# Optimization experiments

Measured on AMD Instinct MI355X. Metric: run time of the kernel, lower is better.

The kernel has to match this reference:

```python
import jax, jax.numpy as jnp
import numpy as np

B, N, D = 64, 1024, 1024

def setup_inputs() -> dict:
    key = jax.random.key(0)
    k1, k2, k3, k4, k5 = jax.random.split(key, 5)
    s = 1.0 / np.sqrt(D)
    return {
        "h_t": jax.random.normal(k1, (B, D), dtype=jnp.float32),
        "keys": jax.random.normal(k2, (B, N, D), dtype=jnp.float32),
        "W_h": jax.random.uniform(k3, (D, D), jnp.float32, -s, s),
        "W_k": jax.random.uniform(k4, (D, D), jnp.float32, -s, s),
        "v": jax.random.uniform(k5, (D,), jnp.float32, -s, s),
    }

def reference(h_t, keys, W_h, W_k, v):
    # W_h(h_t): [B, D]; W_k(keys): [B, N, D]  (nn.Linear computes x @ W.T)
    qh = h_t @ W_h.T                       # [B, D]
    kh = jnp.einsum('bnd,ed->bne', keys, W_k)  # [B, N, D]
    energy = jnp.tanh(qh[:, None, :] + kh)     # [B, N, D]
    scores = jnp.einsum('bnd,d->bn', energy, v)  # [B, N]
    alpha = jax.nn.softmax(scores, axis=-1)      # [B, N]
    context = jnp.einsum('bn,bnd->bd', alpha, keys)  # [B, D]
    return (context, alpha)
```

## Files before the change

### kernel.cpp

```cpp
#include <hip/hip_runtime.h>
#include <math.h>

#define BB 64
#define NN 1024
#define DD 1024

typedef __bf16 bf16x8 __attribute__((ext_vector_type(8)));
typedef float f32x4 __attribute__((ext_vector_type(4)));
typedef unsigned short u16x8 __attribute__((ext_vector_type(8)));

__device__ __forceinline__ float fast_tanh(float x) {
    return 1.f - 2.f / (__expf(2.f * x) + 1.f);
}

__global__ __launch_bounds__(256) void qh_kernel(const float* __restrict__ h_t,
                                                 const float* __restrict__ W_h,
                                                 float* __restrict__ qh,
                                                 float* __restrict__ scores) {
    __shared__ float hs[DD];
    const int b = blockIdx.y;
    const int e = blockIdx.x * 256 + threadIdx.x;
    scores[(blockIdx.y * 4 + blockIdx.x) * 256 + threadIdx.x] = 0.f;
    for (int i = threadIdx.x; i < DD; i += 256) hs[i] = h_t[b * DD + i];
    __syncthreads();
    const float4* wrow = (const float4*)(W_h + (size_t)e * DD);
    float acc = 0.f;
#pragma unroll 4
    for (int k4 = 0; k4 < DD / 4; ++k4) {
        float4 w = wrow[k4];
        acc = fmaf(w.x, hs[4 * k4 + 0], acc);
        acc = fmaf(w.y, hs[4 * k4 + 1], acc);
        acc = fmaf(w.z, hs[4 * k4 + 2], acc);
        acc = fmaf(w.w, hs[4 * k4 + 3], acc);
    }
    qh[b * DD + e] = acc;
}

#define SPAD 40

__device__ __forceinline__ void split16(const float4* __restrict__ src,
                                        unsigned short* hi, unsigned short* lo) {
    float x[16];
    float4 v0 = src[0], v1 = src[1], v2 = src[2], v3 = src[3];
    x[0] = v0.x; x[1] = v0.y; x[2] = v0.z; x[3] = v0.w;
    x[4] = v1.x; x[5] = v1.y; x[6] = v1.z; x[7] = v1.w;
    x[8] = v2.x; x[9] = v2.y; x[10] = v2.z; x[11] = v2.w;
    x[12] = v3.x; x[13] = v3.y; x[14] = v3.z; x[15] = v3.w;
#pragma unroll
    for (int i = 0; i < 16; ++i) {
        unsigned int u = __float_as_uint(x[i]);
        hi[i] = (unsigned short)(u >> 16);
        float hif = __uint_as_float(u & 0xFFFF0000u);
        float lof = x[i] - hif;
        lo[i] = (unsigned short)(__float_as_uint(lof) >> 16);
    }
}

__global__ __launch_bounds__(256, 2) void scores_kernel(const float* __restrict__ keys,
                                                        const float* __restrict__ W_k,
                                                        const float* __restrict__ v,
                                                        const float* __restrict__ qh,
                                                        float* __restrict__ scores) {
    __shared__ unsigned short Ah[128 * SPAD];
    __shared__ unsigned short Al[128 * SPAD];
    __shared__ unsigned short Bh[128 * SPAD];
    __shared__ unsigned short Bl[128 * SPAD];
    __shared__ float vs[128];
    __shared__ float qs[128];
    __shared__ float red[128][2];

    const int tid = threadIdx.x;
    const int cp = blockIdx.x;
    const int rt = blockIdx.y;
    const int b = rt >> 3;
    const int n0 = (rt & 7) * 128;
    const int e0 = cp * 128;

    if (tid < 128) {
        vs[tid] = v[e0 + tid];
        qs[tid] = qh[b * DD + e0 + tid];
    }

    const float* Ag = keys + ((size_t)b * NN + n0) * DD;
    const float* Bg = W_k + (size_t)e0 * DD;

    const int w = tid >> 6;
    const int lane = tid & 63;
    const int wm = w & 1;
    const int we = w >> 1;
    const int lcol = lane & 15;
    const int quad = lane >> 4;

    f32x4 acc[4][4];
#pragma unroll
    for (int mi = 0; mi < 4; ++mi)
#pragma unroll
        for (int ni = 0; ni < 4; ++ni) acc[mi][ni] = (f32x4){0.f, 0.f, 0.f, 0.f};

    const int srow = tid >> 1;
    const int sseg = tid & 1;

    float4 pa[4], pb[4];
    {
        const float4* as = (const float4*)(Ag + (size_t)srow * DD + sseg * 16);
        const float4* bs = (const float4*)(Bg + (size_t)srow * DD + sseg * 16);
#pragma unroll
        for (int i = 0; i < 4; ++i) { pa[i] = as[i]; pb[i] = bs[i]; }
    }

    for (int kt = 0; kt < DD / 32; ++kt) {
        __syncthreads();
        {
            unsigned short hi[16], lo[16];
            split16(pa, hi, lo);
            u16x8* dh = (u16x8*)&Ah[srow * SPAD + sseg * 16];
            u16x8* dl = (u16x8*)&Al[srow * SPAD + sseg * 16];
            dh[0] = *(u16x8*)&hi[0]; dh[1] = *(u16x8*)&hi[8];
            dl[0] = *(u16x8*)&lo[0]; dl[1] = *(u16x8*)&lo[8];
            split16(pb, hi, lo);
            u16x8* eh = (u16x8*)&Bh[srow * SPAD + sseg * 16];
            u16x8* el = (u16x8*)&Bl[srow * SPAD + sseg * 16];
            eh[0] = *(u16x8*)&hi[0]; eh[1] = *(u16x8*)&hi[8];
            el[0] = *(u16x8*)&lo[0]; el[1] = *(u16x8*)&lo[8];
        }
        if (kt + 1 < DD / 32) {
            const int k0 = (kt + 1) * 32;
            const float4* as = (const float4*)(Ag + (size_t)srow * DD + k0 + sseg * 16);
            const float4* bs = (const float4*)(Bg + (size_t)srow * DD + k0 + sseg * 16);
#pragma unroll
            for (int i = 0; i < 4; ++i) { pa[i] = as[i]; pb[i] = bs[i]; }
        }
        __syncthreads();

        bf16x8 ah[4], al[4], bh[4], bl[4];
#pragma unroll
        for (int mi = 0; mi < 4; ++mi) {
            const int r = wm * 64 + mi * 16 + lcol;
            ah[mi] = *(const bf16x8*)&Ah[r * SPAD + quad * 8];
            al[mi] = *(const bf16x8*)&Al[r * SPAD + quad * 8];
        }
#pragma unroll
        for (int ni = 0; ni < 4; ++ni) {
            const int r = we * 64 + ni * 16 + lcol;
            bh[ni] = *(const bf16x8*)&Bh[r * SPAD + quad * 8];
            bl[ni] = *(const bf16x8*)&Bl[r * SPAD + quad * 8];
        }
#pragma unroll
        for (int mi = 0; mi < 4; ++mi)
#pragma unroll
            for (int ni = 0; ni < 4; ++ni) {
                acc[mi][ni] = __builtin_amdgcn_mfma_f32_16x16x32_bf16(ah[mi], bh[ni], acc[mi][ni], 0, 0, 0);
                acc[mi][ni] = __builtin_amdgcn_mfma_f32_16x16x32_bf16(ah[mi], bl[ni], acc[mi][ni], 0, 0, 0);
                acc[mi][ni] = __builtin_amdgcn_mfma_f32_16x16x32_bf16(al[mi], bh[ni], acc[mi][ni], 0, 0, 0);
            }
    }

    float part[4][4];
#pragma unroll
    for (int mi = 0; mi < 4; ++mi)
#pragma unroll
        for (int r = 0; r < 4; ++r) part[mi][r] = 0.f;
#pragma unroll
    for (int mi = 0; mi < 4; ++mi)
#pragma unroll
        for (int ni = 0; ni < 4; ++ni) {
            const int e = we * 64 + ni * 16 + lcol;
            const float vv = vs[e];
            const float qv = qs[e];
#pragma unroll
            for (int r = 0; r < 4; ++r)
                part[mi][r] += vv * fast_tanh(qv + acc[mi][ni][r]);
        }
#pragma unroll
    for (int mi = 0; mi < 4; ++mi)
#pragma unroll
        for (int r = 0; r < 4; ++r) {
            float p = part[mi][r];
            p += __shfl_xor(p, 1);
            p += __shfl_xor(p, 2);
            p += __shfl_xor(p, 4);
            p += __shfl_xor(p, 8);
            if (lcol == 0) red[wm * 64 + mi * 16 + quad * 4 + r][we] = p;
        }
    __syncthreads();
    if (tid < 128) atomicAdd(&scores[b * NN + n0 + tid], red[tid][0] + red[tid][1]);
}

__global__ __launch_bounds__(256) void softmax_kernel(const float* __restrict__ scores,
                                                      float* __restrict__ alpha,
                                                      float* __restrict__ context) {
    const int b = blockIdx.x;
    const int t = threadIdx.x;
#pragma unroll
    for (int j = 0; j < 4; ++j) context[b * DD + t + 256 * j] = 0.f;

    float x[4];
    float m = -1e30f;
#pragma unroll
    for (int j = 0; j < 4; ++j) {
        x[j] = scores[b * NN + t + 256 * j];
        m = fmaxf(m, x[j]);
    }
#pragma unroll
    for (int mask = 32; mask >= 1; mask >>= 1) m = fmaxf(m, __shfl_xor(m, mask));
    __shared__ float wred[4];
    __shared__ float wsum[4];
    const int wv = t >> 6;
    if ((t & 63) == 0) wred[wv] = m;
    __syncthreads();
    m = fmaxf(fmaxf(wred[0], wred[1]), fmaxf(wred[2], wred[3]));
    float s = 0.f;
#pragma unroll
    for (int j = 0; j < 4; ++j) {
        x[j] = expf(x[j] - m);
        s += x[j];
    }
#pragma unroll
    for (int mask = 32; mask >= 1; mask >>= 1) s += __shfl_xor(s, mask);
    if ((t & 63) == 0) wsum[wv] = s;
    __syncthreads();
    s = wsum[0] + wsum[1] + wsum[2] + wsum[3];
    const float inv = 1.f / s;
#pragma unroll
    for (int j = 0; j < 4; ++j) alpha[b * NN + t + 256 * j] = x[j] * inv;
}

__global__ __launch_bounds__(256) void context_kernel(const float* __restrict__ keys,
                                                      const float* __restrict__ alpha,
                                                      float* __restrict__ context) {
    const int b = blockIdx.y;
    const int nc = blockIdx.x;
    const int t = threadIdx.x;
    __shared__ float al[128];
    if (t < 128) al[t] = alpha[b * NN + nc * 128 + t];
    __syncthreads();
    const float4* kp = (const float4*)(keys + ((size_t)b * NN + nc * 128) * DD);
    float4 acc = {0.f, 0.f, 0.f, 0.f};
#pragma unroll 4
    for (int n = 0; n < 128; ++n) {
        const float a = al[n];
        float4 kv = kp[(size_t)n * (DD / 4) + t];
        acc.x = fmaf(a, kv.x, acc.x);
        acc.y = fmaf(a, kv.y, acc.y);
        acc.z = fmaf(a, kv.z, acc.z);
        acc.w = fmaf(a, kv.w, acc.w);
    }
    float* cp = context + b * DD + 4 * t;
    atomicAdd(cp + 0, acc.x);
    atomicAdd(cp + 1, acc.y);
    atomicAdd(cp + 2, acc.z);
    atomicAdd(cp + 3, acc.w);
}

extern "C" void kernel_launch(void* const* d_in, const int* in_sizes, int n_in,
                              void* d_out, int out_size, void* d_ws, size_t ws_size,
                              hipStream_t stream) {
    const float* h_t = (const float*)d_in[0];
    const float* keys = (const float*)d_in[1];
    const float* W_h = (const float*)d_in[2];
    const float* W_k = (const float*)d_in[3];
    const float* v = (const float*)d_in[4];

    float* context = (float*)d_out;
    float* alpha = (float*)d_out + BB * DD;
    float* qh = (float*)d_ws;
    float* scores = (float*)d_ws + BB * DD;

    qh_kernel<<<dim3(4, BB), 256, 0, stream>>>(h_t, W_h, qh, scores);
    scores_kernel<<<dim3(8, 512), 256, 0, stream>>>(keys, W_k, v, qh, scores);
    softmax_kernel<<<BB, 256, 0, stream>>>(scores, alpha, context);
    context_kernel<<<dim3(8, BB), 256, 0, stream>>>(keys, alpha, context);
}
```

Baseline: 754.7 us.

## Pre-convert keys and W_k to tiled fp16 and use single-pass fp16 MFMA

Adds conversion kernels that write keys and W_k as fp16 into a tiled workspace layout. The scores GEMM then streams these tiles into LDS with global_load_lds and needs one fp16 MFMA per tile instead of the three-pass bf16 hi/lo split. Context is also computed from the fp16 copy, and qh computes four batch rows per block so each W_h load is reused. This costs an extra read/write pass over keys and lowers precision to fp16; it only runs when the workspace is large enough (about 128MB), otherwise the old path is kept.

After: 677.1 us. 10.3% less time.

```diff
diff --git a/kernel.cpp b/kernel.cpp
--- a/kernel.cpp
+++ b/kernel.cpp
@@ -6,17 +6,266 @@
 #define DD 1024
 
 typedef __bf16 bf16x8 __attribute__((ext_vector_type(8)));
+typedef _Float16 f16x8 __attribute__((ext_vector_type(8)));
+typedef _Float16 f16x4 __attribute__((ext_vector_type(4)));
 typedef float f32x4 __attribute__((ext_vector_type(4)));
 typedef unsigned short u16x8 __attribute__((ext_vector_type(8)));
 
+#define GLOAD_LDS16(g, l)                                                  \
+    __builtin_amdgcn_global_load_lds(                                      \
+        (const __attribute__((address_space(1))) unsigned int*)(g),        \
+        (__attribute__((address_space(3))) unsigned int*)(l), 16, 0, 0)
+
 __device__ __forceinline__ float fast_tanh(float x) {
     return 1.f - 2.f / (__expf(2.f * x) + 1.f);
 }
 
-__global__ __launch_bounds__(256) void qh_kernel(const float* __restrict__ h_t,
-                                                 const float* __restrict__ W_h,
-                                                 float* __restrict__ qh,
-                                                 float* __restrict__ scores) {
+
+__global__ __launch_bounds__(256) void cvt_keys(const float* __restrict__ keys,
+                                                _Float16* __restrict__ keysT) {
+    const int b = blockIdx.y;
+    const int nt = blockIdx.x;
+    const int t = threadIdx.x;
+    const float4* src = (const float4*)(keys + ((size_t)b * NN + nt * 128) * DD);
+    _Float16* dst = keysT + (((size_t)b * 8 + nt) * 32) * 4096;
+    const int kt = t >> 3;
+    const int kc = (t & 7) * 4;
+    _Float16* dcol = dst + (size_t)kt * 4096 + kc;
+#pragma unroll 4
+    for (int n = 0; n < 128; ++n) {
+        float4 v4 = src[n * 256 + t];
+        f16x4 h = {(_Float16)v4.x, (_Float16)v4.y, (_Float16)v4.z, (_Float16)v4.w};
+        *(f16x4*)(dcol + n * 32) = h;
+    }
+}
+
+__global__ __launch_bounds__(256) void cvt_wk(const float* __restrict__ W_k,
+                                              _Float16* __restrict__ wkT) {
+    const int et = blockIdx.x;
+    const int t = threadIdx.x;
+    const float4* src = (const float4*)(W_k + (size_t)et * 128 * DD);
+    _Float16* dst = wkT + ((size_t)et * 32) * 4096;
+    const int kt = t >> 3;
+    const int kc = (t & 7) * 4;
+    _Float16* dcol = dst + (size_t)kt * 4096 + kc;
+#pragma unroll 4
+    for (int n = 0; n < 128; ++n) {
+        float4 v4 = src[n * 256 + t];
+        f16x4 h = {(_Float16)v4.x, (_Float16)v4.y, (_Float16)v4.z, (_Float16)v4.w};
+        *(f16x4*)(dcol + n * 32) = h;
+    }
+}
+
+__global__ __launch_bounds__(256) void qh_fast(const float* __restrict__ h_t,
+                                               const float* __restrict__ W_h,
+                                               float* __restrict__ qh,
+                                               float* __restrict__ scores) {
+    __shared__ float hs[4 * 1024];
+    const int ec = blockIdx.x;
+    const int bg = blockIdx.y;
+    const int t = threadIdx.x;
+    const int flat = bg * 4 + ec;
+#pragma unroll
+    for (int j = 0; j < 4; ++j) scores[flat * 1024 + j * 256 + t] = 0.f;
+    const float4* hsrc = (const float4*)(h_t + (size_t)bg * 4 * DD);
+    float4* hdst = (float4*)hs;
+    for (int i = t; i < 1024; i += 256) hdst[i] = hsrc[i];
+    __syncthreads();
+    const int e = ec * 256 + t;
+    const float4* wrow = (const float4*)(W_h + (size_t)e * DD);
+    float a0 = 0.f, a1 = 0.f, a2 = 0.f, a3 = 0.f;
+#pragma unroll 2
+    for (int k4 = 0; k4 < 256; ++k4) {
+        float4 wv = wrow[k4];
+        const float* h0 = &hs[4 * k4];
+        a0 = fmaf(wv.x, h0[0], a0); a0 = fmaf(wv.y, h0[1], a0);
+        a0 = fmaf(wv.z, h0[2], a0); a0 = fmaf(wv.w, h0[3], a0);
+        const float* h1 = &hs[1024 + 4 * k4];
+        a1 = fmaf(wv.x, h1[0], a1); a1 = fmaf(wv.y, h1[1], a1);
+        a1 = fmaf(wv.z, h1[2], a1); a1 = fmaf(wv.w, h1[3], a1);
+        const float* h2 = &hs[2048 + 4 * k4];
+        a2 = fmaf(wv.x, h2[0], a2); a2 = fmaf(wv.y, h2[1], a2);
+        a2 = fmaf(wv.z, h2[2], a2); a2 = fmaf(wv.w, h2[3], a2);
+        const float* h3 = &hs[3072 + 4 * k4];
+        a3 = fmaf(wv.x, h3[0], a3); a3 = fmaf(wv.y, h3[1], a3);
+        a3 = fmaf(wv.z, h3[2], a3); a3 = fmaf(wv.w, h3[3], a3);
+    }
+    const int b0 = bg * 4;
+    qh[(b0 + 0) * DD + e] = a0;
+    qh[(b0 + 1) * DD + e] = a1;
+    qh[(b0 + 2) * DD + e] = a2;
+    qh[(b0 + 3) * DD + e] = a3;
+}
+
+__global__ __launch_bounds__(256) void scores_mfma(const _Float16* __restrict__ keysT,
+                                                   const _Float16* __restrict__ wkT,
+                                                   const float* __restrict__ v,
+                                                   const float* __restrict__ qh,
+                                                   float* __restrict__ scores) {
+    __shared__ _Float16 As[128 * 32];
+    __shared__ _Float16 Bs[128 * 32];
+    __shared__ float vs[128];
+    __shared__ float qs[128];
+    __shared__ float red[128][2];
+
+    const int tid = threadIdx.x;
+    const int cp = blockIdx.x;
+    const int rt = blockIdx.y;
+    const int b = rt >> 3;
+    const int nt = rt & 7;
+    const int e0 = cp * 128;
+
+    if (tid < 128) {
+        vs[tid] = v[e0 + tid];
+        qs[tid] = qh[b * DD + e0 + tid];
+    }
+
+    const char* Abase = (const char*)(keysT + (((size_t)b * 8 + nt) * 32) * 4096);
+    const char* Bbase = (const char*)(wkT + ((size_t)cp * 32) * 4096);
+
+    const int w = tid >> 6;
+    const int lane = tid & 63;
+    const int wm = w & 1;
+    const int we = w >> 1;
+    const int lcol = lane & 15;
+    const int quad = lane >> 4;
+    const int soff = w * 2048 + lane * 16;
+
+    f32x4 acc[4][4];
+#pragma unroll
+    for (int mi = 0; mi < 4; ++mi)
+#pragma unroll
+        for (int ni = 0; ni < 4; ++ni) acc[mi][ni] = (f32x4){0.f, 0.f, 0.f, 0.f};
+
+    for (int kt = 0; kt < 32; ++kt) {
+        __syncthreads();
+        const char* ag = Abase + (size_t)kt * 8192 + soff;
+        const char* bg = Bbase + (size_t)kt * 8192 + soff;
+        char* al_ = (char*)As + soff;
+        char* bl_ = (char*)Bs + soff;
+        GLOAD_LDS16(ag, al_);
+        GLOAD_LDS16(ag + 1024, al_ + 1024);
+        GLOAD_LDS16(bg, bl_);
+        GLOAD_LDS16(bg + 1024, bl_ + 1024);
+        __syncthreads();
+
+        f16x8 af[4], bf[4];
+#pragma unroll
+        for (int mi = 0; mi < 4; ++mi)
+            af[mi] = *(const f16x8*)&As[(wm * 64 + mi * 16 + lcol) * 32 + quad * 8];
+#pragma unroll
+        for (int ni = 0; ni < 4; ++ni)
+            bf[ni] = *(const f16x8*)&Bs[(we * 64 + ni * 16 + lcol) * 32 + quad * 8];
+#pragma unroll
+        for (int mi = 0; mi < 4; ++mi)
+#pragma unroll
+            for (int ni = 0; ni < 4; ++ni)
+                acc[mi][ni] = __builtin_amdgcn_mfma_f32_16x16x32_f16(af[mi], bf[ni], acc[mi][ni], 0, 0, 0);
+    }
+
+    float part[4][4];
+#pragma unroll
+    for (int mi = 0; mi < 4; ++mi)
+#pragma unroll
+        for (int r = 0; r < 4; ++r) part[mi][r] = 0.f;
+#pragma unroll
+    for (int mi = 0; mi < 4; ++mi)
+#pragma unroll
+        for (int ni = 0; ni < 4; ++ni) {
+            const int e = we * 64 + ni * 16 + lcol;
+            const float vv = vs[e];
+            const float qv = qs[e];
+#pragma unroll
+            for (int r = 0; r < 4; ++r)
+                part[mi][r] += vv * fast_tanh(qv + acc[mi][ni][r]);
+        }
+#pragma unroll
+    for (int mi = 0; mi < 4; ++mi)
+#pragma unroll
+        for (int r = 0; r < 4; ++r) {
+            float p = part[mi][r];
+            p += __shfl_xor(p, 1);
+            p += __shfl_xor(p, 2);
+            p += __shfl_xor(p, 4);
+            p += __shfl_xor(p, 8);
+            if (lcol == 0) red[wm * 64 + mi * 16 + quad * 4 + r][we] = p;
+        }
+    __syncthreads();
+    if (tid < 128) atomicAdd(&scores[b * NN + nt * 128 + tid], red[tid][0] + red[tid][1]);
+}
+
+__global__ __launch_bounds__(256) void softmax_kernel(const float* __restrict__ scores,
+                                                      float* __restrict__ alpha,
+                                                      float* __restrict__ context) {
+    const int b = blockIdx.x;
+    const int t = threadIdx.x;
+#pragma unroll
+    for (int j = 0; j < 4; ++j) context[b * DD + t + 256 * j] = 0.f;
+    float x[4];
+    float m = -1e30f;
+#pragma unroll
+    for (int j = 0; j < 4; ++j) {
+        x[j] = scores[b * NN + t + 256 * j];
+        m = fmaxf(m, x[j]);
+    }
+#pragma unroll
+    for (int mask = 32; mask >= 1; mask >>= 1) m = fmaxf(m, __shfl_xor(m, mask));
+    __shared__ float wred[4];
+    __shared__ float wsum[4];
+    const int wv = t >> 6;
+    if ((t & 63) == 0) wred[wv] = m;
+    __syncthreads();
+    m = fmaxf(fmaxf(wred[0], wred[1]), fmaxf(wred[2], wred[3]));
+    float s = 0.f;
+#pragma unroll
+    for (int j = 0; j < 4; ++j) {
+        x[j] = expf(x[j] - m);
+        s += x[j];
+    }
+#pragma unroll
+    for (int mask = 32; mask >= 1; mask >>= 1) s += __shfl_xor(s, mask);
+    if ((t & 63) == 0) wsum[wv] = s;
+    __syncthreads();
+    s = wsum[0] + wsum[1] + wsum[2] + wsum[3];
+    const float inv = 1.f / s;
+#pragma unroll
+    for (int j = 0; j < 4; ++j) alpha[b * NN + t + 256 * j] = x[j] * inv;
+}
+
+__global__ __launch_bounds__(256) void context_f16(const _Float16* __restrict__ keysT,
+                                                   const float* __restrict__ alpha,
+                                                   float* __restrict__ context) {
+    const int b = blockIdx.y;
+    const int nc = blockIdx.x;
+    const int t = threadIdx.x;
+    __shared__ float al[128];
+    if (t < 128) al[t] = alpha[b * NN + nc * 128 + t];
+    __syncthreads();
+    const _Float16* chunk = keysT + (((size_t)b * 8 + nc) * 32) * 4096;
+    const int kt = t >> 3;
+    const int kc = (t & 7) * 4;
+    const _Float16* p = chunk + (size_t)kt * 4096 + kc;
+    float4 acc = {0.f, 0.f, 0.f, 0.f};
+#pragma unroll 4
+    for (int n = 0; n < 128; ++n) {
+        const float a = al[n];
+        f16x4 kv = *(const f16x4*)(p + n * 32);
+        acc.x = fmaf(a, (float)kv[0], acc.x);
+        acc.y = fmaf(a, (float)kv[1], acc.y);
+        acc.z = fmaf(a, (float)kv[2], acc.z);
+        acc.w = fmaf(a, (float)kv[3], acc.w);
+    }
+    float* cp = context + b * DD + kt * 32 + kc;
+    atomicAdd(cp + 0, acc.x);
+    atomicAdd(cp + 1, acc.y);
+    atomicAdd(cp + 2, acc.z);
+    atomicAdd(cp + 3, acc.w);
+}
+
+__global__ __launch_bounds__(256) void qh_fb(const float* __restrict__ h_t,
+                                             const float* __restrict__ W_h,
+                                             float* __restrict__ qh,
+                                             float* __restrict__ scores) {
     __shared__ float hs[DD];
     const int b = blockIdx.y;
     const int e = blockIdx.x * 256 + threadIdx.x;
@@ -37,7 +286,6 @@
 }
 
 #define SPAD 40
-
 __device__ __forceinline__ void split16(const float4* __restrict__ src,
                                         unsigned short* hi, unsigned short* lo) {
     float x[16];
@@ -56,11 +304,11 @@
     }
 }
 
-__global__ __launch_bounds__(256, 2) void scores_kernel(const float* __restrict__ keys,
-                                                        const float* __restrict__ W_k,
-                                                        const float* __restrict__ v,
-                                                        const float* __restrict__ qh,
-                                                        float* __restrict__ scores) {
+__global__ __launch_bounds__(256, 2) void scores_fb(const float* __restrict__ keys,
+                                                    const float* __restrict__ W_k,
+                                                    const float* __restrict__ v,
+                                                    const float* __restrict__ qh,
+                                                    float* __restrict__ scores) {
     __shared__ unsigned short Ah[128 * SPAD];
     __shared__ unsigned short Al[128 * SPAD];
     __shared__ unsigned short Bh[128 * SPAD];
@@ -75,31 +323,25 @@
     const int b = rt >> 3;
     const int n0 = (rt & 7) * 128;
     const int e0 = cp * 128;
-
     if (tid < 128) {
         vs[tid] = v[e0 + tid];
         qs[tid] = qh[b * DD + e0 + tid];
     }
-
     const float* Ag = keys + ((size_t)b * NN + n0) * DD;
     const float* Bg = W_k + (size_t)e0 * DD;
-
     const int w = tid >> 6;
     const int lane = tid & 63;
     const int wm = w & 1;
     const int we = w >> 1;
     const int lcol = lane & 15;
     const int quad = lane >> 4;
-
     f32x4 acc[4][4];
 #pragma unroll
     for (int mi = 0; mi < 4; ++mi)
 #pragma unroll
         for (int ni = 0; ni < 4; ++ni) acc[mi][ni] = (f32x4){0.f, 0.f, 0.f, 0.f};
-
     const int srow = tid >> 1;
     const int sseg = tid & 1;
-
     float4 pa[4], pb[4];
     {
         const float4* as = (const float4*)(Ag + (size_t)srow * DD + sseg * 16);
@@ -107,7 +349,6 @@
 #pragma unroll
         for (int i = 0; i < 4; ++i) { pa[i] = as[i]; pb[i] = bs[i]; }
     }
-
     for (int kt = 0; kt < DD / 32; ++kt) {
         __syncthreads();
         {
@@ -131,30 +372,28 @@
             for (int i = 0; i < 4; ++i) { pa[i] = as[i]; pb[i] = bs[i]; }
         }
         __syncthreads();
-
-        bf16x8 ah[4], al[4], bh[4], bl[4];
+        bf16x8 ah[4], al2[4], bh[4], bl2[4];
 #pragma unroll
         for (int mi = 0; mi < 4; ++mi) {
             const int r = wm * 64 + mi * 16 + lcol;
             ah[mi] = *(const bf16x8*)&Ah[r * SPAD + quad * 8];
-            al[mi] = *(const bf16x8*)&Al[r * SPAD + quad * 8];
+            al2[mi] = *(const bf16x8*)&Al[r * SPAD + quad * 8];
         }
 #pragma unroll
         for (int ni = 0; ni < 4; ++ni) {
             const int r = we * 64 + ni * 16 + lcol;
             bh[ni] = *(const bf16x8*)&Bh[r * SPAD + quad * 8];
-            bl[ni] = *(const bf16x8*)&Bl[r * SPAD + quad * 8];
+            bl2[ni] = *(const bf16x8*)&Bl[r * SPAD + quad * 8];
         }
 #pragma unroll
         for (int mi = 0; mi < 4; ++mi)
 #pragma unroll
             for (int ni = 0; ni < 4; ++ni) {
                 acc[mi][ni] = __builtin_amdgcn_mfma_f32_16x16x32_bf16(ah[mi], bh[ni], acc[mi][ni], 0, 0, 0);
-                acc[mi][ni] = __builtin_amdgcn_mfma_f32_16x16x32_bf16(ah[mi], bl[ni], acc[mi][ni], 0, 0, 0);
-                acc[mi][ni] = __builtin_amdgcn_mfma_f32_16x16x32_bf16(al[mi], bh[ni], acc[mi][ni], 0, 0, 0);
+                acc[mi][ni] = __builtin_amdgcn_mfma_f32_16x16x32_bf16(ah[mi], bl2[ni], acc[mi][ni], 0, 0, 0);
+                acc[mi][ni] = __builtin_amdgcn_mfma_f32_16x16x32_bf16(al2[mi], bh[ni], acc[mi][ni], 0, 0, 0);
             }
     }
-
     float part[4][4];
 #pragma unroll
     for (int mi = 0; mi < 4; ++mi)
@@ -186,48 +425,9 @@
     if (tid < 128) atomicAdd(&scores[b * NN + n0 + tid], red[tid][0] + red[tid][1]);
 }
 
-__global__ __launch_bounds__(256) void softmax_kernel(const float* __restrict__ scores,
-                                                      float* __restrict__ alpha,
-                                                      float* __restrict__ context) {
-    const int b = blockIdx.x;
-    const int t = threadIdx.x;
-#pragma unroll
-    for (int j = 0; j < 4; ++j) context[b * DD + t + 256 * j] = 0.f;
-
-    float x[4];
-    float m = -1e30f;
-#pragma unroll
-    for (int j = 0; j < 4; ++j) {
-        x[j] = scores[b * NN + t + 256 * j];
-        m = fmaxf(m, x[j]);
-    }
-#pragma unroll
-    for (int mask = 32; mask >= 1; mask >>= 1) m = fmaxf(m, __shfl_xor(m, mask));
-    __shared__ float wred[4];
-    __shared__ float wsum[4];
-    const int wv = t >> 6;
-    if ((t & 63) == 0) wred[wv] = m;
-    __syncthreads();
-    m = fmaxf(fmaxf(wred[0], wred[1]), fmaxf(wred[2], wred[3]));
-    float s = 0.f;
-#pragma unroll
-    for (int j = 0; j < 4; ++j) {
-        x[j] = expf(x[j] - m);
-        s += x[j];
-    }
-#pragma unroll
-    for (int mask = 32; mask >= 1; mask >>= 1) s += __shfl_xor(s, mask);
-    if ((t & 63) == 0) wsum[wv] = s;
-    __syncthreads();
-    s = wsum[0] + wsum[1] + wsum[2] + wsum[3];
-    const float inv = 1.f / s;
-#pragma unroll
-    for (int j = 0; j < 4; ++j) alpha[b * NN + t + 256 * j] = x[j] * inv;
-}
-
-__global__ __launch_bounds__(256) void context_kernel(const float* __restrict__ keys,
-                                                      const float* __restrict__ alpha,
-                                                      float* __restrict__ context) {
+__global__ __launch_bounds__(256) void context_fb(const float* __restrict__ keys,
+                                                  const float* __restrict__ alpha,
+                                                  float* __restrict__ context) {
     const int b = blockIdx.y;
     const int nc = blockIdx.x;
     const int t = threadIdx.x;
@@ -266,8 +466,23 @@
     float* qh = (float*)d_ws;
     float* scores = (float*)d_ws + BB * DD;
 
-    qh_kernel<<<dim3(4, BB), 256, 0, stream>>>(h_t, W_h, qh, scores);
-    scores_kernel<<<dim3(8, 512), 256, 0, stream>>>(keys, W_k, v, qh, scores);
-    softmax_kernel<<<BB, 256, 0, stream>>>(scores, alpha, context);
-    context_kernel<<<dim3(8, BB), 256, 0, stream>>>(keys, alpha, context);
-}
+    const size_t wkT_off = (size_t)2 * BB * DD * sizeof(float);
+    const size_t keysT_off = wkT_off + (size_t)DD * DD * 2;
+    const size_t need = keysT_off + (size_t)BB * NN * DD * 2;
+
+    if (ws_size >= need) {
+        _Float16* wkT = (_Float16*)((char*)d_ws + wkT_off);
+        _Float16* keysT = (_Float16*)((char*)d_ws + keysT_off);
+        cvt_keys<<<dim3(8, BB), 256, 0, stream>>>(keys, keysT);
+        cvt_wk<<<dim3(8), 256, 0, stream>>>(W_k, wkT);
+        qh_fast<<<dim3(4, 16), 256, 0, stream>>>(h_t, W_h, qh, scores);
+        scores_mfma<<<dim3(8, 512), 256, 0, stream>>>(keysT, wkT, v, qh, scores);
+        softmax_kernel<<<BB, 256, 0, stream>>>(scores, alpha, context);
+        context_f16<<<dim3(8, BB), 256, 0, stream>>>(keysT, alpha, context);
+    } else {
+        qh_fb<<<dim3(4, BB), 256, 0, stream>>>(h_t, W_h, qh, scores);
+        scores_fb<<<dim3(8, 512), 256, 0, stream>>>(keys, W_k, v, qh, scores);
+        softmax_kernel<<<BB, 256, 0, stream>>>(scores, alpha, context);
+        context_fb<<<dim3(8, BB), 256, 0, stream>>>(keys, alpha, context);
+    }
+}
```
